# Optimization experiments

Hardware: AMD Instinct MI355X
Metric: run time of the kernel (lower is better)

Reference implementation:

```python
import jax, jax.numpy as jnp
import numpy as np

M, K, N = 8192, 4096, 4096
ALPHA, BETA = 0.002, 0.0005


def setup_inputs() -> dict:
    key = jax.random.key(0)
    kx, kw, kb = jax.random.split(key, 3)
    # int8-range quantized activations and weights (stored as int32 for portability)
    x = jax.random.randint(kx, (M, K), -127, 127, dtype=jnp.int32)
    weight = jax.random.randint(kw, (N, K), -127, 127, dtype=jnp.int32)  # (out, in)
    bias = jax.random.randint(kb, (1, N), -(2**20), 2**20, dtype=jnp.int32)
    alpha = jnp.float32(ALPHA)
    beta = jnp.float32(BETA)
    return {"x": x, "weight": weight, "bias": bias, "alpha": alpha, "beta": beta}


def reference(x, weight, bias, alpha, beta):
    # int8 GEMM with int32 accumulation: acc[m, n] = sum_k x[m, k] * W[n, k]
    acc = jnp.matmul(x, weight.T, preferred_element_type=jnp.int32)  # [M, N] int32
    # CUTLASS-style epilogue: D = round(alpha * acc + beta * bias) -> int32
    y = alpha * acc.astype(jnp.float32) + beta * bias.astype(jnp.float32)
    return jnp.round(y).astype(jnp.int32)
```

## Files before the change

kernel.cpp:

```cpp
#include <hip/hip_runtime.h>
#include <hip/hip_bf16.h>
#include <stdint.h>

#define M_DIM 8192
#define N_DIM 4096
#define K_DIM 4096

#define BM 256
#define BN 256
#define BK 64
#define NT (K_DIM / BK)
#define DEPTH 4

typedef int v4i __attribute__((ext_vector_type(4)));

#define AS1C(p) ((const __attribute__((address_space(1))) void*)(p))
#define AS3(p)  ((__attribute__((address_space(3))) void*)(p))

__device__ __forceinline__ int pack4(int a, int b, int c, int d) {
  return (a & 0xff) | ((b & 0xff) << 8) | ((c & 0xff) << 16) | (d << 24);
}

__global__ void pack_i8_kernel(const int* __restrict__ in, char* __restrict__ out,
                               int nchunks) {
  int idx = blockIdx.x * blockDim.x + threadIdx.x;
  int stride = gridDim.x * blockDim.x;
  const int4* pin = (const int4*)in;
  int4* pout = (int4*)out;
  for (int i = idx; i < nchunks; i += stride) {
    int4 v0 = pin[4 * i + 0];
    int4 v1 = pin[4 * i + 1];
    int4 v2 = pin[4 * i + 2];
    int4 v3 = pin[4 * i + 3];
    int4 o;
    o.x = pack4(v0.x, v0.y, v0.z, v0.w);
    o.y = pack4(v1.x, v1.y, v1.z, v1.w);
    o.z = pack4(v2.x, v2.y, v2.z, v2.w);
    o.w = pack4(v3.x, v3.y, v3.z, v3.w);
    pout[i] = o;
  }
}

__global__ __launch_bounds__(512, 2) void gemm_i8_kernel(
    const char* __restrict__ A8, const char* __restrict__ B8,
    const int* __restrict__ bias, const float* __restrict__ alpha_p,
    const float* __restrict__ beta_p, int* __restrict__ out) {
  __shared__ alignas(16) char lds[DEPTH][BM * BK + BN * BK];

  const int tid  = threadIdx.x;
  const int lane = tid & 63;
  const int wave = tid >> 6;

  const int orig = blockIdx.x;
  const int swz  = (orig & 7) * (512 / 8) + (orig >> 3);
  const int bm   = (swz >> 4) * BM;
  const int bn   = (swz & 15) * BN;

  int aoff[2], boff[2], ldsoff[2];
#pragma unroll
  for (int i = 0; i < 2; ++i) {
    int linear = i * 8192 + tid * 16;
    int row = linear >> 6;
    int p   = (linear >> 4) & 3;
    int g   = p ^ ((row >> 1) & 3);
    ldsoff[i] = i * 8192 + wave * 1024;
    aoff[i] = (bm + row) * K_DIM + g * 16;
    boff[i] = (bn + row) * K_DIM + g * 16;
  }

#define STAGE(t)                                                                    \
  do {                                                                              \
    const char* ab_ = A8 + (t) * BK;                                                \
    const char* bb_ = B8 + (t) * BK;                                                \
    char* base_ = &lds[(t) & (DEPTH - 1)][0];                                       \
    _Pragma("unroll") for (int i_ = 0; i_ < 2; ++i_) {                              \
      __builtin_amdgcn_global_load_lds(AS1C(ab_ + aoff[i_]),                        \
                                       AS3(base_ + ldsoff[i_]), 16, 0, 0);          \
      __builtin_amdgcn_global_load_lds(AS1C(bb_ + boff[i_]),                        \
                                       AS3(base_ + 16384 + ldsoff[i_]), 16, 0, 0);  \
    }                                                                               \
  } while (0)

  v4i acc[8][4];
#pragma unroll
  for (int i = 0; i < 8; ++i)
#pragma unroll
    for (int j = 0; j < 4; ++j) acc[i][j] = (v4i){0, 0, 0, 0};

  const int wr = wave >> 2;
  const int wc = wave & 3;
  const int frow = lane & 15;
  const int swzoff = ((lane >> 4) ^ ((frow >> 1) & 3)) << 4;

#define COMPUTE(t)                                                                  \
  do {                                                                              \
    const char* base_ = &lds[(t) & (DEPTH - 1)][0];                                 \
    const char* As_ = base_;                                                        \
    const char* Bs_ = base_ + 16384;                                                \
    v4i bf[4];                                                                      \
    _Pragma("unroll") for (int nj = 0; nj < 4; ++nj) {                              \
      int r_ = wc * 64 + nj * 16 + frow;                                            \
      bf[nj] = *(const v4i*)(Bs_ + r_ * 64 + swzoff);                               \
    }                                                                               \
    __builtin_amdgcn_s_setprio(1);                                                  \
    _Pragma("unroll") for (int mi = 0; mi < 8; ++mi) {                              \
      int r_ = wr * 128 + mi * 16 + frow;                                           \
      v4i af_ = *(const v4i*)(As_ + r_ * 64 + swzoff);                              \
      _Pragma("unroll") for (int nj = 0; nj < 4; ++nj)                              \
        acc[mi][nj] = __builtin_amdgcn_mfma_i32_16x16x64_i8(af_, bf[nj],            \
                                                            acc[mi][nj], 0, 0, 0); \
    }                                                                               \
    __builtin_amdgcn_s_setprio(0);                                                  \
  } while (0)

  STAGE(0);
  STAGE(1);
  STAGE(2);

  for (int t = 0; t < NT - 2; ++t) {
    asm volatile("s_waitcnt vmcnt(8) lgkmcnt(0)" ::: "memory");
    __builtin_amdgcn_s_barrier();
    if (t + 3 < NT) STAGE(t + 3);
    COMPUTE(t);
  }
  asm volatile("s_waitcnt vmcnt(4) lgkmcnt(0)" ::: "memory");
  __builtin_amdgcn_s_barrier();
  COMPUTE(NT - 2);
  asm volatile("s_waitcnt vmcnt(0) lgkmcnt(0)" ::: "memory");
  __builtin_amdgcn_s_barrier();
  COMPUTE(NT - 1);

  const float alpha = *alpha_p;
  const float beta  = *beta_p;
  const int col0 = bn + wc * 64 + frow;
  float bb4[4];
#pragma unroll
  for (int nj = 0; nj < 4; ++nj) bb4[nj] = beta * (float)bias[col0 + nj * 16];

  const int rbase = bm + wr * 128 + (lane >> 4) * 4;
#pragma unroll
  for (int mi = 0; mi < 8; ++mi) {
#pragma unroll
    for (int r = 0; r < 4; ++r) {
      size_t rowoff = (size_t)(rbase + mi * 16 + r) * N_DIM;
#pragma unroll
      for (int nj = 0; nj < 4; ++nj) {
        out[rowoff + col0 + nj * 16] =
            (int)rintf(fmaf(alpha, (float)acc[mi][nj][r], bb4[nj]));
      }
    }
  }
#undef STAGE
#undef COMPUTE
}

__global__ void naive_kernel(const int* __restrict__ x, const int* __restrict__ w,
                             const int* __restrict__ bias,
                             const float* __restrict__ alpha_p,
                             const float* __restrict__ beta_p,
                             int* __restrict__ out) {
  size_t idx = (size_t)blockIdx.x * 256 + threadIdx.x;
  int m = (int)(idx / N_DIM);
  int n = (int)(idx % N_DIM);
  const int4* xr = (const int4*)(x + (size_t)m * K_DIM);
  const int4* wr = (const int4*)(w + (size_t)n * K_DIM);
  int acc = 0;
  for (int k = 0; k < K_DIM / 4; ++k) {
    int4 a = xr[k];
    int4 b = wr[k];
    acc += a.x * b.x + a.y * b.y + a.z * b.z + a.w * b.w;
  }
  out[idx] = (int)rintf(fmaf(*alpha_p, (float)acc, (*beta_p) * (float)bias[n]));
}

extern "C" void kernel_launch(void* const* d_in, const int* in_sizes, int n_in,
                              void* d_out, int out_size, void* d_ws, size_t ws_size,
                              hipStream_t stream) {
  const int*   x     = (const int*)d_in[0];
  const int*   w     = (const int*)d_in[1];
  const int*   bias  = (const int*)d_in[2];
  const float* alpha = (const float*)d_in[3];
  const float* beta  = (const float*)d_in[4];
  int* out = (int*)d_out;

  const size_t a8_bytes = (size_t)M_DIM * K_DIM;
  const size_t b8_bytes = (size_t)N_DIM * K_DIM;

  if (ws_size >= a8_bytes + b8_bytes) {
    char* A8 = (char*)d_ws;
    char* B8 = A8 + a8_bytes;
    pack_i8_kernel<<<2048, 256, 0, stream>>>(x, A8, (int)(a8_bytes / 16));
    pack_i8_kernel<<<2048, 256, 0, stream>>>(w, B8, (int)(b8_bytes / 16));
    const int nblk = (M_DIM / BM) * (N_DIM / BN);
    gemm_i8_kernel<<<nblk, 512, 0, stream>>>(A8, B8, bias, alpha, beta, out);
  } else {
    naive_kernel<<<(M_DIM * (size_t)N_DIM) / 256, 256, 0, stream>>>(x, w, bias, alpha, beta, out);
  }
}
```

Baseline: 186.2 us.

## Switch to 32x32x32 int8 MFMA, split K-step staging, fuse pack kernels

```diff
diff --git a/kernel.cpp b/kernel.cpp
--- a/kernel.cpp
+++ b/kernel.cpp
@@ -12,7 +12,8 @@
 #define NT (K_DIM / BK)
 #define DEPTH 4
 
-typedef int v4i __attribute__((ext_vector_type(4)));
+typedef int v4i  __attribute__((ext_vector_type(4)));
+typedef int v16i __attribute__((ext_vector_type(16)));
 
 #define AS1C(p) ((const __attribute__((address_space(1))) void*)(p))
 #define AS3(p)  ((__attribute__((address_space(3))) void*)(p))
@@ -21,23 +22,32 @@
   return (a & 0xff) | ((b & 0xff) << 8) | ((c & 0xff) << 16) | (d << 24);
 }
 
-__global__ void pack_i8_kernel(const int* __restrict__ in, char* __restrict__ out,
-                               int nchunks) {
+__global__ void pack_both_kernel(const int* __restrict__ x, const int* __restrict__ w,
+                                 char* __restrict__ A8, char* __restrict__ B8,
+                                 int nA, int nTot) {
   int idx = blockIdx.x * blockDim.x + threadIdx.x;
   int stride = gridDim.x * blockDim.x;
-  const int4* pin = (const int4*)in;
-  int4* pout = (int4*)out;
-  for (int i = idx; i < nchunks; i += stride) {
-    int4 v0 = pin[4 * i + 0];
-    int4 v1 = pin[4 * i + 1];
-    int4 v2 = pin[4 * i + 2];
-    int4 v3 = pin[4 * i + 3];
+  for (int i = idx; i < nTot; i += stride) {
+    const int4* pin;
+    int4* pout;
+    if (i < nA) {
+      pin  = (const int4*)x + 4 * (size_t)i;
+      pout = (int4*)A8 + i;
+    } else {
+      int j = i - nA;
+      pin  = (const int4*)w + 4 * (size_t)j;
+      pout = (int4*)B8 + j;
+    }
+    int4 v0 = pin[0];
+    int4 v1 = pin[1];
+    int4 v2 = pin[2];
+    int4 v3 = pin[3];
     int4 o;
     o.x = pack4(v0.x, v0.y, v0.z, v0.w);
     o.y = pack4(v1.x, v1.y, v1.z, v1.w);
     o.z = pack4(v2.x, v2.y, v2.z, v2.w);
     o.w = pack4(v3.x, v3.y, v3.z, v3.w);
-    pout[i] = o;
+    *pout = o;
   }
 }
 
@@ -68,90 +78,114 @@
     boff[i] = (bn + row) * K_DIM + g * 16;
   }
 
-#define STAGE(t)                                                                    \
+#define STAGE_A(t)                                                                  \
   do {                                                                              \
     const char* ab_ = A8 + (t) * BK;                                                \
+    char* base_ = &lds[(t) & (DEPTH - 1)][0];                                       \
+    _Pragma("unroll") for (int i_ = 0; i_ < 2; ++i_)                                \
+      __builtin_amdgcn_global_load_lds(AS1C(ab_ + aoff[i_]),                        \
+                                       AS3(base_ + ldsoff[i_]), 16, 0, 0);          \
+  } while (0)
+
+#define STAGE_B(t)                                                                  \
+  do {                                                                              \
     const char* bb_ = B8 + (t) * BK;                                                \
     char* base_ = &lds[(t) & (DEPTH - 1)][0];                                       \
-    _Pragma("unroll") for (int i_ = 0; i_ < 2; ++i_) {                              \
-      __builtin_amdgcn_global_load_lds(AS1C(ab_ + aoff[i_]),                        \
-                                       AS3(base_ + ldsoff[i_]), 16, 0, 0);          \
+    _Pragma("unroll") for (int i_ = 0; i_ < 2; ++i_)                                \
       __builtin_amdgcn_global_load_lds(AS1C(bb_ + boff[i_]),                        \
                                        AS3(base_ + 16384 + ldsoff[i_]), 16, 0, 0);  \
-    }                                                                               \
   } while (0)
 
-  v4i acc[8][4];
-#pragma unroll
-  for (int i = 0; i < 8; ++i)
-#pragma unroll
-    for (int j = 0; j < 4; ++j) acc[i][j] = (v4i){0, 0, 0, 0};
+  v16i acc[4][2];
+#pragma unroll
+  for (int i = 0; i < 4; ++i)
+#pragma unroll
+    for (int j = 0; j < 2; ++j)
+#pragma unroll
+      for (int r = 0; r < 16; ++r) acc[i][j][r] = 0;
 
   const int wr = wave >> 2;
   const int wc = wave & 3;
-  const int frow = lane & 15;
-  const int swzoff = ((lane >> 4) ^ ((frow >> 1) & 3)) << 4;
-
-#define COMPUTE(t)                                                                  \
+  const int l31   = lane & 31;
+  const int khalf = lane >> 5;
+  const int kxor  = (l31 >> 1) & 3;
+
+#define COMPUTE_KS(t, ks)                                                           \
   do {                                                                              \
     const char* base_ = &lds[(t) & (DEPTH - 1)][0];                                 \
     const char* As_ = base_;                                                        \
     const char* Bs_ = base_ + 16384;                                                \
-    v4i bf[4];                                                                      \
-    _Pragma("unroll") for (int nj = 0; nj < 4; ++nj) {                              \
-      int r_ = wc * 64 + nj * 16 + frow;                                            \
-      bf[nj] = *(const v4i*)(Bs_ + r_ * 64 + swzoff);                               \
-    }                                                                               \
+    const int coff_ = ((((ks) * 2 + khalf) ^ kxor) << 4);                           \
+    v4i bf0 = *(const v4i*)(Bs_ + (wc * 64 + 0 * 32 + l31) * 64 + coff_);           \
+    v4i bf1 = *(const v4i*)(Bs_ + (wc * 64 + 1 * 32 + l31) * 64 + coff_);           \
+    v4i af0 = *(const v4i*)(As_ + (wr * 128 + 0 * 32 + l31) * 64 + coff_);          \
+    v4i af1 = *(const v4i*)(As_ + (wr * 128 + 1 * 32 + l31) * 64 + coff_);          \
+    v4i af2 = *(const v4i*)(As_ + (wr * 128 + 2 * 32 + l31) * 64 + coff_);          \
+    v4i af3 = *(const v4i*)(As_ + (wr * 128 + 3 * 32 + l31) * 64 + coff_);          \
+    asm volatile("s_waitcnt lgkmcnt(0)" ::: "memory");                              \
     __builtin_amdgcn_s_setprio(1);                                                  \
-    _Pragma("unroll") for (int mi = 0; mi < 8; ++mi) {                              \
-      int r_ = wr * 128 + mi * 16 + frow;                                           \
-      v4i af_ = *(const v4i*)(As_ + r_ * 64 + swzoff);                              \
-      _Pragma("unroll") for (int nj = 0; nj < 4; ++nj)                              \
-        acc[mi][nj] = __builtin_amdgcn_mfma_i32_16x16x64_i8(af_, bf[nj],            \
-                                                            acc[mi][nj], 0, 0, 0); \
-    }                                                                               \
+    acc[0][0] = __builtin_amdgcn_mfma_i32_32x32x32_i8(af0, bf0, acc[0][0], 0, 0, 0);\
+    acc[1][0] = __builtin_amdgcn_mfma_i32_32x32x32_i8(af1, bf0, acc[1][0], 0, 0, 0);\
+    acc[2][0] = __builtin_amdgcn_mfma_i32_32x32x32_i8(af2, bf0, acc[2][0], 0, 0, 0);\
+    acc[3][0] = __builtin_amdgcn_mfma_i32_32x32x32_i8(af3, bf0, acc[3][0], 0, 0, 0);\
+    acc[0][1] = __builtin_amdgcn_mfma_i32_32x32x32_i8(af0, bf1, acc[0][1], 0, 0, 0);\
+    acc[1][1] = __builtin_amdgcn_mfma_i32_32x32x32_i8(af1, bf1, acc[1][1], 0, 0, 0);\
+    acc[2][1] = __builtin_amdgcn_mfma_i32_32x32x32_i8(af2, bf1, acc[2][1], 0, 0, 0);\
+    acc[3][1] = __builtin_amdgcn_mfma_i32_32x32x32_i8(af3, bf1, acc[3][1], 0, 0, 0);\
     __builtin_amdgcn_s_setprio(0);                                                  \
   } while (0)
 
-  STAGE(0);
-  STAGE(1);
-  STAGE(2);
+  STAGE_A(0); STAGE_B(0);
+  STAGE_A(1); STAGE_B(1);
+  STAGE_A(2); STAGE_B(2);
 
   for (int t = 0; t < NT - 2; ++t) {
     asm volatile("s_waitcnt vmcnt(8) lgkmcnt(0)" ::: "memory");
     __builtin_amdgcn_s_barrier();
-    if (t + 3 < NT) STAGE(t + 3);
-    COMPUTE(t);
+    if (t + 3 < NT) STAGE_A(t + 3);
+    COMPUTE_KS(t, 0);
+    __builtin_amdgcn_s_barrier();
+    if (t + 3 < NT) STAGE_B(t + 3);
+    COMPUTE_KS(t, 1);
   }
   asm volatile("s_waitcnt vmcnt(4) lgkmcnt(0)" ::: "memory");
   __builtin_amdgcn_s_barrier();
-  COMPUTE(NT - 2);
+  COMPUTE_KS(NT - 2, 0);
+  __builtin_amdgcn_s_barrier();
+  COMPUTE_KS(NT - 2, 1);
   asm volatile("s_waitcnt vmcnt(0) lgkmcnt(0)" ::: "memory");
   __builtin_amdgcn_s_barrier();
-  COMPUTE(NT - 1);
+  COMPUTE_KS(NT - 1, 0);
+  __builtin_amdgcn_s_barrier();
+  COMPUTE_KS(NT - 1, 1);
 
   const float alpha = *alpha_p;
   const float beta  = *beta_p;
-  const int col0 = bn + wc * 64 + frow;
-  float bb4[4];
-#pragma unroll
-  for (int nj = 0; nj < 4; ++nj) bb4[nj] = beta * (float)bias[col0 + nj * 16];
-
-  const int rbase = bm + wr * 128 + (lane >> 4) * 4;
-#pragma unroll
-  for (int mi = 0; mi < 8; ++mi) {
-#pragma unroll
-    for (int r = 0; r < 4; ++r) {
-      size_t rowoff = (size_t)(rbase + mi * 16 + r) * N_DIM;
-#pragma unroll
-      for (int nj = 0; nj < 4; ++nj) {
-        out[rowoff + col0 + nj * 16] =
-            (int)rintf(fmaf(alpha, (float)acc[mi][nj][r], bb4[nj]));
+  const int col0 = bn + wc * 64 + l31;
+  float bb2[2];
+#pragma unroll
+  for (int nj = 0; nj < 2; ++nj) bb2[nj] = beta * (float)bias[col0 + nj * 32];
+
+  const int rbase = bm + wr * 128 + 4 * khalf;
+#pragma unroll
+  for (int mi = 0; mi < 4; ++mi) {
+#pragma unroll
+    for (int q = 0; q < 4; ++q) {
+#pragma unroll
+      for (int rr = 0; rr < 4; ++rr) {
+        int reg = q * 4 + rr;
+        size_t rowoff = (size_t)(rbase + mi * 32 + rr + 8 * q) * N_DIM;
+#pragma unroll
+        for (int nj = 0; nj < 2; ++nj) {
+          out[rowoff + col0 + nj * 32] =
+              (int)rintf(fmaf(alpha, (float)acc[mi][nj][reg], bb2[nj]));
+        }
       }
     }
   }
-#undef STAGE
-#undef COMPUTE
+#undef STAGE_A
+#undef STAGE_B
+#undef COMPUTE_KS
 }
 
 __global__ void naive_kernel(const int* __restrict__ x, const int* __restrict__ w,
@@ -189,8 +223,9 @@
   if (ws_size >= a8_bytes + b8_bytes) {
     char* A8 = (char*)d_ws;
     char* B8 = A8 + a8_bytes;
-    pack_i8_kernel<<<2048, 256, 0, stream>>>(x, A8, (int)(a8_bytes / 16));
-    pack_i8_kernel<<<2048, 256, 0, stream>>>(w, B8, (int)(b8_bytes / 16));
+    const int nA = (int)(a8_bytes / 16);
+    const int nTot = (int)((a8_bytes + b8_bytes) / 16);
+    pack_both_kernel<<<2048, 256, 0, stream>>>(x, w, A8, B8, nA, nTot);
     const int nblk = (M_DIM / BM) * (N_DIM / BN);
     gemm_i8_kernel<<<nblk, 512, 0, stream>>>(A8, B8, bias, alpha, beta, out);
   } else {
```

New measurement: 202.6 us. 1.09x slower.

## Split GEMM k-step into two barrier-separated phases and fuse pack kernels

Applied to the files above, without the earlier changes.

```diff
diff --git a/kernel.cpp b/kernel.cpp
--- a/kernel.cpp
+++ b/kernel.cpp
@@ -21,23 +21,32 @@
   return (a & 0xff) | ((b & 0xff) << 8) | ((c & 0xff) << 16) | (d << 24);
 }
 
-__global__ void pack_i8_kernel(const int* __restrict__ in, char* __restrict__ out,
-                               int nchunks) {
+__global__ void pack_both_kernel(const int* __restrict__ x, const int* __restrict__ w,
+                                 char* __restrict__ A8, char* __restrict__ B8,
+                                 int nA, int nTot) {
   int idx = blockIdx.x * blockDim.x + threadIdx.x;
   int stride = gridDim.x * blockDim.x;
-  const int4* pin = (const int4*)in;
-  int4* pout = (int4*)out;
-  for (int i = idx; i < nchunks; i += stride) {
-    int4 v0 = pin[4 * i + 0];
-    int4 v1 = pin[4 * i + 1];
-    int4 v2 = pin[4 * i + 2];
-    int4 v3 = pin[4 * i + 3];
+  for (int i = idx; i < nTot; i += stride) {
+    const int4* pin;
+    int4* pout;
+    if (i < nA) {
+      pin  = (const int4*)x + 4 * (size_t)i;
+      pout = (int4*)A8 + i;
+    } else {
+      int j = i - nA;
+      pin  = (const int4*)w + 4 * (size_t)j;
+      pout = (int4*)B8 + j;
+    }
+    int4 v0 = pin[0];
+    int4 v1 = pin[1];
+    int4 v2 = pin[2];
+    int4 v3 = pin[3];
     int4 o;
     o.x = pack4(v0.x, v0.y, v0.z, v0.w);
     o.y = pack4(v1.x, v1.y, v1.z, v1.w);
     o.z = pack4(v2.x, v2.y, v2.z, v2.w);
     o.w = pack4(v3.x, v3.y, v3.z, v3.w);
-    pout[i] = o;
+    *pout = o;
   }
 }
 
@@ -68,17 +77,22 @@
     boff[i] = (bn + row) * K_DIM + g * 16;
   }
 
-#define STAGE(t)                                                                    \
+#define STAGE_A(t)                                                                  \
   do {                                                                              \
     const char* ab_ = A8 + (t) * BK;                                                \
+    char* base_ = &lds[(t) & (DEPTH - 1)][0];                                       \
+    _Pragma("unroll") for (int i_ = 0; i_ < 2; ++i_)                                \
+      __builtin_amdgcn_global_load_lds(AS1C(ab_ + aoff[i_]),                        \
+                                       AS3(base_ + ldsoff[i_]), 16, 0, 0);          \
+  } while (0)
+
+#define STAGE_B(t)                                                                  \
+  do {                                                                              \
     const char* bb_ = B8 + (t) * BK;                                                \
     char* base_ = &lds[(t) & (DEPTH - 1)][0];                                       \
-    _Pragma("unroll") for (int i_ = 0; i_ < 2; ++i_) {                              \
-      __builtin_amdgcn_global_load_lds(AS1C(ab_ + aoff[i_]),                        \
-                                       AS3(base_ + ldsoff[i_]), 16, 0, 0);          \
+    _Pragma("unroll") for (int i_ = 0; i_ < 2; ++i_)                                \
       __builtin_amdgcn_global_load_lds(AS1C(bb_ + boff[i_]),                        \
                                        AS3(base_ + 16384 + ldsoff[i_]), 16, 0, 0);  \
-    }                                                                               \
   } while (0)
 
   v4i acc[8][4];
@@ -90,45 +104,76 @@
   const int wr = wave >> 2;
   const int wc = wave & 3;
   const int frow = lane & 15;
-  const int swzoff = ((lane >> 4) ^ ((frow >> 1) & 3)) << 4;
-
-#define COMPUTE(t)                                                                  \
-  do {                                                                              \
+  const int fchunk = lane >> 4;
+  const int swzoff = ((fchunk ^ ((frow >> 1) & 3)) << 4);
+
+  STAGE_A(0); STAGE_B(0);
+  STAGE_A(1); STAGE_B(1);
+  STAGE_A(2); STAGE_B(2);
+
+#define PH0(t, DO_STAGE)                                                            \
+  do {                                                                              \
+    if (DO_STAGE) STAGE_A((t) + 3);                                                 \
     const char* base_ = &lds[(t) & (DEPTH - 1)][0];                                 \
-    const char* As_ = base_;                                                        \
-    const char* Bs_ = base_ + 16384;                                                \
-    v4i bf[4];                                                                      \
     _Pragma("unroll") for (int nj = 0; nj < 4; ++nj) {                              \
       int r_ = wc * 64 + nj * 16 + frow;                                            \
-      bf[nj] = *(const v4i*)(Bs_ + r_ * 64 + swzoff);                               \
+      bf[nj] = *(const v4i*)(base_ + 16384 + r_ * 64 + swzoff);                     \
+    }                                                                               \
+    v4i af_[4];                                                                     \
+    _Pragma("unroll") for (int mi = 0; mi < 4; ++mi) {                              \
+      int r_ = wr * 128 + mi * 16 + frow;                                           \
+      af_[mi] = *(const v4i*)(base_ + r_ * 64 + swzoff);                            \
     }                                                                               \
     __builtin_amdgcn_s_setprio(1);                                                  \
-    _Pragma("unroll") for (int mi = 0; mi < 8; ++mi) {                              \
-      int r_ = wr * 128 + mi * 16 + frow;                                           \
-      v4i af_ = *(const v4i*)(As_ + r_ * 64 + swzoff);                              \
+    _Pragma("unroll") for (int mi = 0; mi < 4; ++mi)                                \
       _Pragma("unroll") for (int nj = 0; nj < 4; ++nj)                              \
-        acc[mi][nj] = __builtin_amdgcn_mfma_i32_16x16x64_i8(af_, bf[nj],            \
+        acc[mi][nj] = __builtin_amdgcn_mfma_i32_16x16x64_i8(af_[mi], bf[nj],        \
                                                             acc[mi][nj], 0, 0, 0); \
+    __builtin_amdgcn_s_setprio(0);                                                  \
+  } while (0)
+
+#define PH1(t, DO_STAGE)                                                            \
+  do {                                                                              \
+    if (DO_STAGE) STAGE_B((t) + 3);                                                 \
+    const char* base_ = &lds[(t) & (DEPTH - 1)][0];                                 \
+    v4i af_[4];                                                                     \
+    _Pragma("unroll") for (int mi = 0; mi < 4; ++mi) {                              \
+      int r_ = wr * 128 + (mi + 4) * 16 + frow;                                     \
+      af_[mi] = *(const v4i*)(base_ + r_ * 64 + swzoff);                            \
     }                                                                               \
+    __builtin_amdgcn_s_setprio(1);                                                  \
+    _Pragma("unroll") for (int mi = 0; mi < 4; ++mi)                                \
+      _Pragma("unroll") for (int nj = 0; nj < 4; ++nj)                              \
+        acc[mi + 4][nj] = __builtin_amdgcn_mfma_i32_16x16x64_i8(af_[mi], bf[nj],    \
+                                                            acc[mi + 4][nj],       \
+                                                            0, 0, 0);              \
     __builtin_amdgcn_s_setprio(0);                                                  \
   } while (0)
 
-  STAGE(0);
-  STAGE(1);
-  STAGE(2);
-
   for (int t = 0; t < NT - 2; ++t) {
+    v4i bf[4];
     asm volatile("s_waitcnt vmcnt(8) lgkmcnt(0)" ::: "memory");
     __builtin_amdgcn_s_barrier();
-    if (t + 3 < NT) STAGE(t + 3);
-    COMPUTE(t);
-  }
-  asm volatile("s_waitcnt vmcnt(4) lgkmcnt(0)" ::: "memory");
-  __builtin_amdgcn_s_barrier();
-  COMPUTE(NT - 2);
-  asm volatile("s_waitcnt vmcnt(0) lgkmcnt(0)" ::: "memory");
-  __builtin_amdgcn_s_barrier();
-  COMPUTE(NT - 1);
+    PH0(t, t + 3 < NT);
+    __builtin_amdgcn_s_barrier();
+    PH1(t, t + 3 < NT);
+  }
+  {
+    v4i bf[4];
+    asm volatile("s_waitcnt vmcnt(4) lgkmcnt(0)" ::: "memory");
+    __builtin_amdgcn_s_barrier();
+    PH0(NT - 2, false);
+    __builtin_amdgcn_s_barrier();
+    PH1(NT - 2, false);
+  }
+  {
+    v4i bf[4];
+    asm volatile("s_waitcnt vmcnt(0) lgkmcnt(0)" ::: "memory");
+    __builtin_amdgcn_s_barrier();
+    PH0(NT - 1, false);
+    __builtin_amdgcn_s_barrier();
+    PH1(NT - 1, false);
+  }
 
   const float alpha = *alpha_p;
   const float beta  = *beta_p;
@@ -150,8 +195,10 @@
       }
     }
   }
-#undef STAGE
-#undef COMPUTE
+#undef STAGE_A
+#undef STAGE_B
+#undef PH0
+#undef PH1
 }
 
 __global__ void naive_kernel(const int* __restrict__ x, const int* __restrict__ w,
@@ -189,8 +236,9 @@
   if (ws_size >= a8_bytes + b8_bytes) {
     char* A8 = (char*)d_ws;
     char* B8 = A8 + a8_bytes;
-    pack_i8_kernel<<<2048, 256, 0, stream>>>(x, A8, (int)(a8_bytes / 16));
-    pack_i8_kernel<<<2048, 256, 0, stream>>>(w, B8, (int)(b8_bytes / 16));
+    const int nA = (int)(a8_bytes / 16);
+    const int nTot = (int)((a8_bytes + b8_bytes) / 16);
+    pack_both_kernel<<<2048, 256, 0, stream>>>(x, w, A8, B8, nA, nTot);
     const int nblk = (M_DIM / BM) * (N_DIM / BN);
     gemm_i8_kernel<<<nblk, 512, 0, stream>>>(A8, B8, bias, alpha, beta, out);
   } else {
```

Measured after the change: 183.6 us. No clear change (-1.4%).

## Shrink GEMM tile to 128x256 with 4 waves, triple buffering, fused pack kernel

Applied to the files above, without the earlier changes.

```diff
diff --git a/kernel.cpp b/kernel.cpp
--- a/kernel.cpp
+++ b/kernel.cpp
@@ -6,11 +6,12 @@
 #define N_DIM 4096
 #define K_DIM 4096
 
-#define BM 256
+#define BM 128
 #define BN 256
 #define BK 64
 #define NT (K_DIM / BK)
-#define DEPTH 4
+#define DEPTH 3
+#define TILE_LDS (BM * BK + BN * BK)
 
 typedef int v4i __attribute__((ext_vector_type(4)));
 
@@ -21,112 +22,123 @@
   return (a & 0xff) | ((b & 0xff) << 8) | ((c & 0xff) << 16) | (d << 24);
 }
 
-__global__ void pack_i8_kernel(const int* __restrict__ in, char* __restrict__ out,
-                               int nchunks) {
+__global__ void pack_both_kernel(const int* __restrict__ x, const int* __restrict__ w,
+                                 char* __restrict__ A8, char* __restrict__ B8,
+                                 int nA, int nTot) {
   int idx = blockIdx.x * blockDim.x + threadIdx.x;
   int stride = gridDim.x * blockDim.x;
-  const int4* pin = (const int4*)in;
-  int4* pout = (int4*)out;
-  for (int i = idx; i < nchunks; i += stride) {
-    int4 v0 = pin[4 * i + 0];
-    int4 v1 = pin[4 * i + 1];
-    int4 v2 = pin[4 * i + 2];
-    int4 v3 = pin[4 * i + 3];
+  for (int i = idx; i < nTot; i += stride) {
+    const int4* pin;
+    int4* pout;
+    if (i < nA) {
+      pin  = (const int4*)x + 4 * (size_t)i;
+      pout = (int4*)A8 + i;
+    } else {
+      int j = i - nA;
+      pin  = (const int4*)w + 4 * (size_t)j;
+      pout = (int4*)B8 + j;
+    }
+    int4 v0 = pin[0];
+    int4 v1 = pin[1];
+    int4 v2 = pin[2];
+    int4 v3 = pin[3];
     int4 o;
     o.x = pack4(v0.x, v0.y, v0.z, v0.w);
     o.y = pack4(v1.x, v1.y, v1.z, v1.w);
     o.z = pack4(v2.x, v2.y, v2.z, v2.w);
     o.w = pack4(v3.x, v3.y, v3.z, v3.w);
-    pout[i] = o;
-  }
-}
-
-__global__ __launch_bounds__(512, 2) void gemm_i8_kernel(
+    *pout = o;
+  }
+}
+
+__global__ __launch_bounds__(256, 2) void gemm_i8_kernel(
     const char* __restrict__ A8, const char* __restrict__ B8,
     const int* __restrict__ bias, const float* __restrict__ alpha_p,
     const float* __restrict__ beta_p, int* __restrict__ out) {
-  __shared__ alignas(16) char lds[DEPTH][BM * BK + BN * BK];
+  __shared__ alignas(16) char lds[DEPTH][TILE_LDS];
 
   const int tid  = threadIdx.x;
   const int lane = tid & 63;
   const int wave = tid >> 6;
 
   const int orig = blockIdx.x;
-  const int swz  = (orig & 7) * (512 / 8) + (orig >> 3);
-  const int bm   = (swz >> 4) * BM;
-  const int bn   = (swz & 15) * BN;
-
-  int aoff[2], boff[2], ldsoff[2];
+  const int swz  = (orig & 7) * (1024 / 8) + (orig >> 3);
+  const int bm   = (swz & 63) * BM;
+  const int bn   = (swz >> 6) * BN;
+
+  int aoff[2], boff[4], ldsoffA[2], ldsoffB[4];
 #pragma unroll
   for (int i = 0; i < 2; ++i) {
-    int linear = i * 8192 + tid * 16;
+    int linear = i * 4096 + tid * 16;
     int row = linear >> 6;
     int p   = (linear >> 4) & 3;
     int g   = p ^ ((row >> 1) & 3);
-    ldsoff[i] = i * 8192 + wave * 1024;
+    ldsoffA[i] = i * 4096 + wave * 1024;
     aoff[i] = (bm + row) * K_DIM + g * 16;
-    boff[i] = (bn + row) * K_DIM + g * 16;
+  }
+#pragma unroll
+  for (int j = 0; j < 4; ++j) {
+    int linear = j * 4096 + tid * 16;
+    int row = linear >> 6;
+    int p   = (linear >> 4) & 3;
+    int g   = p ^ ((row >> 1) & 3);
+    ldsoffB[j] = BM * BK + j * 4096 + wave * 1024;
+    boff[j] = (bn + row) * K_DIM + g * 16;
   }
 
 #define STAGE(t)                                                                    \
   do {                                                                              \
     const char* ab_ = A8 + (t) * BK;                                                \
     const char* bb_ = B8 + (t) * BK;                                                \
-    char* base_ = &lds[(t) & (DEPTH - 1)][0];                                       \
-    _Pragma("unroll") for (int i_ = 0; i_ < 2; ++i_) {                              \
+    char* base_ = &lds[(t) % DEPTH][0];                                             \
+    _Pragma("unroll") for (int i_ = 0; i_ < 2; ++i_)                                \
       __builtin_amdgcn_global_load_lds(AS1C(ab_ + aoff[i_]),                        \
-                                       AS3(base_ + ldsoff[i_]), 16, 0, 0);          \
-      __builtin_amdgcn_global_load_lds(AS1C(bb_ + boff[i_]),                        \
-                                       AS3(base_ + 16384 + ldsoff[i_]), 16, 0, 0);  \
+                                       AS3(base_ + ldsoffA[i_]), 16, 0, 0);         \
+    _Pragma("unroll") for (int j_ = 0; j_ < 4; ++j_)                                \
+      __builtin_amdgcn_global_load_lds(AS1C(bb_ + boff[j_]),                        \
+                                       AS3(base_ + ldsoffB[j_]), 16, 0, 0);         \
+  } while (0)
+
+  v4i acc[8][4];
+#pragma unroll
+  for (int i = 0; i < 8; ++i)
+#pragma unroll
+    for (int j = 0; j < 4; ++j) acc[i][j] = (v4i){0, 0, 0, 0};
+
+  const int wc = wave;
+  const int frow = lane & 15;
+  const int fchunk = lane >> 4;
+  const int swzoff = ((fchunk ^ ((frow >> 1) & 3)) << 4);
+
+#define COMPUTE(t)                                                                  \
+  do {                                                                              \
+    const char* base_ = &lds[(t) % DEPTH][0];                                       \
+    v4i bf_[4];                                                                     \
+    _Pragma("unroll") for (int nj = 0; nj < 4; ++nj)                                \
+      bf_[nj] = *(const v4i*)(base_ + BM * BK +                                     \
+                              (wc * 64 + nj * 16 + frow) * 64 + swzoff);            \
+    _Pragma("unroll") for (int mi = 0; mi < 8; ++mi) {                              \
+      v4i af_ = *(const v4i*)(base_ + (mi * 16 + frow) * 64 + swzoff);              \
+      __builtin_amdgcn_s_setprio(1);                                                \
+      _Pragma("unroll") for (int nj = 0; nj < 4; ++nj)                              \
+        acc[mi][nj] = __builtin_amdgcn_mfma_i32_16x16x64_i8(af_, bf_[nj],           \
+                                                            acc[mi][nj], 0, 0, 0); \
+      __builtin_amdgcn_s_setprio(0);                                                \
     }                                                                               \
   } while (0)
 
-  v4i acc[8][4];
-#pragma unroll
-  for (int i = 0; i < 8; ++i)
-#pragma unroll
-    for (int j = 0; j < 4; ++j) acc[i][j] = (v4i){0, 0, 0, 0};
-
-  const int wr = wave >> 2;
-  const int wc = wave & 3;
-  const int frow = lane & 15;
-  const int swzoff = ((lane >> 4) ^ ((frow >> 1) & 3)) << 4;
-
-#define COMPUTE(t)                                                                  \
-  do {                                                                              \
-    const char* base_ = &lds[(t) & (DEPTH - 1)][0];                                 \
-    const char* As_ = base_;                                                        \
-    const char* Bs_ = base_ + 16384;                                                \
-    v4i bf[4];                                                                      \
-    _Pragma("unroll") for (int nj = 0; nj < 4; ++nj) {                              \
-      int r_ = wc * 64 + nj * 16 + frow;                                            \
-      bf[nj] = *(const v4i*)(Bs_ + r_ * 64 + swzoff);                               \
-    }                                                                               \
-    __builtin_amdgcn_s_setprio(1);                                                  \
-    _Pragma("unroll") for (int mi = 0; mi < 8; ++mi) {                              \
-      int r_ = wr * 128 + mi * 16 + frow;                                           \
-      v4i af_ = *(const v4i*)(As_ + r_ * 64 + swzoff);                              \
-      _Pragma("unroll") for (int nj = 0; nj < 4; ++nj)                              \
-        acc[mi][nj] = __builtin_amdgcn_mfma_i32_16x16x64_i8(af_, bf[nj],            \
-                                                            acc[mi][nj], 0, 0, 0); \
-    }                                                                               \
-    __builtin_amdgcn_s_setprio(0);                                                  \
-  } while (0)
-
   STAGE(0);
   STAGE(1);
-  STAGE(2);
-
-  for (int t = 0; t < NT - 2; ++t) {
-    asm volatile("s_waitcnt vmcnt(8) lgkmcnt(0)" ::: "memory");
+
+  for (int t = 0; t < NT - 1; ++t) {
+    if (t < NT - 1 - 1 + 1) {
+      asm volatile("s_waitcnt vmcnt(6)" ::: "memory");
+    }
     __builtin_amdgcn_s_barrier();
-    if (t + 3 < NT) STAGE(t + 3);
+    if (t + 2 < NT) STAGE(t + 2);
     COMPUTE(t);
   }
-  asm volatile("s_waitcnt vmcnt(4) lgkmcnt(0)" ::: "memory");
-  __builtin_amdgcn_s_barrier();
-  COMPUTE(NT - 2);
-  asm volatile("s_waitcnt vmcnt(0) lgkmcnt(0)" ::: "memory");
+  asm volatile("s_waitcnt vmcnt(0)" ::: "memory");
   __builtin_amdgcn_s_barrier();
   COMPUTE(NT - 1);
 
@@ -137,7 +149,7 @@
 #pragma unroll
   for (int nj = 0; nj < 4; ++nj) bb4[nj] = beta * (float)bias[col0 + nj * 16];
 
-  const int rbase = bm + wr * 128 + (lane >> 4) * 4;
+  const int rbase = bm + (lane >> 4) * 4;
 #pragma unroll
   for (int mi = 0; mi < 8; ++mi) {
 #pragma unroll
@@ -189,10 +201,11 @@
   if (ws_size >= a8_bytes + b8_bytes) {
     char* A8 = (char*)d_ws;
     char* B8 = A8 + a8_bytes;
-    pack_i8_kernel<<<2048, 256, 0, stream>>>(x, A8, (int)(a8_bytes / 16));
-    pack_i8_kernel<<<2048, 256, 0, stream>>>(w, B8, (int)(b8_bytes / 16));
+    const int nA = (int)(a8_bytes / 16);
+    const int nTot = (int)((a8_bytes + b8_bytes) / 16);
+    pack_both_kernel<<<2048, 256, 0, stream>>>(x, w, A8, B8, nA, nTot);
     const int nblk = (M_DIM / BM) * (N_DIM / BN);
-    gemm_i8_kernel<<<nblk, 512, 0, stream>>>(A8, B8, bias, alpha, beta, out);
+    gemm_i8_kernel<<<nblk, 256, 0, stream>>>(A8, B8, bias, alpha, beta, out);
   } else {
     naive_kernel<<<(M_DIM * (size_t)N_DIM) / 256, 256, 0, stream>>>(x, w, bias, alpha, beta, out);
   }
```

Measured after the change: 201.5 us. +8.2%, slower.
